# Optimization experiments

Hardware: AMD Instinct MI355X
Metric: run time of the kernel (lower is better)

Reference implementation:

```python
import jax, jax.numpy as jnp
import numpy as np

H = W = 256
FX = FY = 1.0
CX = CY = 0.5


def setup_inputs() -> dict:
    key = jax.random.key(0)
    k1, k2, k3 = jax.random.split(key, 3)
    B, N = 8, 500000
    points = jax.random.normal(k1, (B, N, 3), dtype=jnp.float32)
    densities = jax.random.uniform(k2, (B, N, 1), dtype=jnp.float32)
    depth = jax.random.uniform(k3, (B, 1, H, W), dtype=jnp.float32)
    return {"points": points, "densities": densities, "depth": depth}


def project_points_to_depth(points, densities):
    # points: [B,N,3], densities: [B,N,1] -> depth grid [B,1,H,W]
    B, N, _ = points.shape
    x = points[:, :, 0]
    y = points[:, :, 1]
    z = points[:, :, 2]
    # pinhole projection; .long() in torch truncates toward zero, as does astype(int32)
    u = jnp.clip(((FX * x / z + CX) * W).astype(jnp.int32), 0, W - 1)  # [B,N]
    v = jnp.clip(((FY * y / z + CY) * H).astype(jnp.int32), 0, H - 1)  # [B,N]
    d = densities[:, :, 0]
    val = jnp.where(d > 0.5, z * d, jnp.float32(0.0))  # conditional contribution
    idx = v * W + u  # flat pixel index [B,N]
    flat = jnp.zeros((B, H * W), dtype=points.dtype)
    flat = flat.at[jnp.arange(B)[:, None], idx].add(val)  # batched scatter-add
    return flat.reshape(B, 1, H, W)


def reference(points, densities, depth):
    projected = project_points_to_depth(points, densities)
    mask = projected > 0
    diff2 = jnp.where(mask, (projected - depth) ** 2, jnp.float32(0.0))
    count = jnp.maximum(jnp.sum(mask), 1)
    # F.mse_loss over masked elements == mean of squared diffs where mask
    return jnp.sum(diff2) / count.astype(diff2.dtype)
```

## Files before the change

### kernel.cpp

```cpp
#include <hip/hip_runtime.h>

#define HH 256
#define WW 256
#define HWSZ (HH * WW)

#define GRIDX 128
#define NSLOTS 1022

__global__ __launch_bounds__(256, 4) void scatter_k(
    const float* __restrict__ pts, const float* __restrict__ dens,
    float* __restrict__ flat, int N)
{
    __shared__ float lds[NSLOTS];
    for (int s = threadIdx.x; s < NSLOTS; s += 256) lds[s] = 0.0f;
    __syncthreads();

    int b = blockIdx.y;
    const float* pb = pts + (size_t)b * N * 3;
    const float* db = dens + (size_t)b * N;
    float* out = flat + (size_t)b * HWSZ;

    int ngroups = N >> 2;
    int gpb = (ngroups + GRIDX - 1) / GRIDX;
    int gbase = blockIdx.x * gpb;
    int gend = min(gbase + gpb, ngroups);
    int nit = (gpb + 255) >> 8;
    int last = ngroups - 1;
    const float4* p4 = (const float4*)pb;
    const float4* d4 = (const float4*)db;

    float corner[4] = {0.0f, 0.0f, 0.0f, 0.0f};

    auto proc = [&](const float4& a, const float4& bb, const float4& c,
                    const float4& dd) {
        float xs[4] = {a.x, a.w, bb.z, c.y};
        float ys[4] = {a.y, bb.x, bb.w, c.z};
        float zs[4] = {a.z, bb.y, c.x, c.w};
        float ds[4] = {dd.x, dd.y, dd.z, dd.w};

        #pragma unroll
        for (int k = 0; k < 4; k++) {
            float d = ds[k];
            float z = zs[k];
            bool acc = d > 0.5f;
            float r = __builtin_amdgcn_rcpf(z) * 256.0f;
            float uf = fmaf(xs[k], r, 128.0f);
            float vf = fmaf(ys[k], r, 128.0f);
            int u = (int)fminf(fmaxf(uf, 0.0f), 255.0f);
            int v = (int)fminf(fmaxf(vf, 0.0f), 255.0f);
            float val = z * d;

            bool u0 = (u == 0), u255 = (u == 255);
            bool v0 = (v == 0), v255 = (v == 255);
            bool ub = u0 | u255;
            bool vb = v0 | v255;
            bool iscorner = acc & ub & vb;
            bool isborder = acc & (ub ^ vb);
            bool isinter  = acc & !ub & !vb;

            int ci = (v255 ? 2 : 0) | (u255 ? 1 : 0);
            corner[0] += (iscorner && ci == 0) ? val : 0.0f;
            corner[1] += (iscorner && ci == 1) ? val : 0.0f;
            corner[2] += (iscorner && ci == 2) ? val : 0.0f;
            corner[3] += (iscorner && ci == 3) ? val : 0.0f;

            int slot = v0 ? u : (v255 ? 256 + u : (u0 ? 511 + v : 767 + v));
            if (isborder) atomicAdd(&lds[slot], val);
            if (isinter)  atomicAdd(out + v * WW + u, val);
        }
    };

    int g = gbase + threadIdx.x;
    int gc = min(g, last);
    float4 A  = p4[3 * gc];
    float4 Bv = p4[3 * gc + 1];
    float4 C  = p4[3 * gc + 2];
    float4 D  = d4[gc];
    if (g >= gend) { D.x = D.y = D.z = D.w = 0.0f; }

    for (int it = 0; it < nit; ++it) {
        int gn = g + 256;
        int gnc = min(gn, last);
        float4 nA  = p4[3 * gnc];
        float4 nB  = p4[3 * gnc + 1];
        float4 nC  = p4[3 * gnc + 2];
        float4 nD  = d4[gnc];
        if (gn >= gend) { nD.x = nD.y = nD.z = nD.w = 0.0f; }

        proc(A, Bv, C, D);

        A = nA; Bv = nB; C = nC; D = nD;
        g = gn;
    }

    #pragma unroll
    for (int j = 0; j < 4; j++) {
        float v = corner[j];
        #pragma unroll
        for (int off = 32; off > 0; off >>= 1) v += __shfl_down(v, off);
        if ((threadIdx.x & 63) == 0) {
            const int cslot[4] = {0, 255, 256, 511};
            atomicAdd(&lds[cslot[j]], v);
        }
    }

    __syncthreads();
    for (int s = threadIdx.x; s < NSLOTS; s += 256) {
        float v = lds[s];
        if (v != 0.0f) {
            int u, vv;
            if (s < 256)      { vv = 0;        u = s; }
            else if (s < 512) { vv = 255;      u = s - 256; }
            else if (s < 768) { u = 0;         vv = s - 512 + 1; }
            else              { u = 255;       vv = s - 768 + 1; }
            atomicAdd(out + vv * WW + u, v);
        }
    }
}

#define LBLOCKS 128
#define ELEMS_PER_THREAD 4
__global__ __launch_bounds__(256) void loss_k(
    const float* __restrict__ flat, const float* __restrict__ depth,
    float* __restrict__ accum, int* __restrict__ done,
    float* __restrict__ out, int total4, int nblocks)
{
    const float4* f4 = (const float4*)flat;
    const float4* z4 = (const float4*)depth;

    int i0 = blockIdx.x * blockDim.x + threadIdx.x;
    int stride = gridDim.x * blockDim.x;

    float4 p[ELEMS_PER_THREAD], q[ELEMS_PER_THREAD];
    bool ok[ELEMS_PER_THREAD];
    #pragma unroll
    for (int k = 0; k < ELEMS_PER_THREAD; k++) {
        int i = i0 + k * stride;
        ok[k] = i < total4;
        if (ok[k]) { p[k] = f4[i]; q[k] = z4[i]; }
    }
    float s = 0.0f;
    int c = 0;
    for (int i = i0 + ELEMS_PER_THREAD * stride; i < total4; i += stride) {
        float4 pp = f4[i];
        float4 qq = z4[i];
        if (pp.x > 0.0f) { float df = pp.x - qq.x; s += df * df; c++; }
        if (pp.y > 0.0f) { float df = pp.y - qq.y; s += df * df; c++; }
        if (pp.z > 0.0f) { float df = pp.z - qq.z; s += df * df; c++; }
        if (pp.w > 0.0f) { float df = pp.w - qq.w; s += df * df; c++; }
    }
    #pragma unroll
    for (int k = 0; k < ELEMS_PER_THREAD; k++) {
        if (ok[k]) {
            float4 pp = p[k], qq = q[k];
            if (pp.x > 0.0f) { float df = pp.x - qq.x; s += df * df; c++; }
            if (pp.y > 0.0f) { float df = pp.y - qq.y; s += df * df; c++; }
            if (pp.z > 0.0f) { float df = pp.z - qq.z; s += df * df; c++; }
            if (pp.w > 0.0f) { float df = pp.w - qq.w; s += df * df; c++; }
        }
    }

    #pragma unroll
    for (int off = 32; off > 0; off >>= 1) {
        s += __shfl_down(s, off);
        c += __shfl_down(c, off);
    }

    __shared__ float bsum[4];
    __shared__ int bcnt[4];
    int wave = threadIdx.x >> 6;
    if ((threadIdx.x & 63) == 0) { bsum[wave] = s; bcnt[wave] = c; }
    __syncthreads();
    if (threadIdx.x == 0) {
        float ts = bsum[0] + bsum[1] + bsum[2] + bsum[3];
        int tc = bcnt[0] + bcnt[1] + bcnt[2] + bcnt[3];
        atomicAdd(accum, ts);
        atomicAdd((int*)accum + 1, tc);
        __threadfence();
        int old = atomicAdd(done, 1);
        if (old == nblocks - 1) {
            float fs = atomicAdd(accum, 0.0f);
            int fc = atomicAdd((int*)accum + 1, 0);
            out[0] = fs / (float)(fc >= 1 ? fc : 1);
        }
    }
}

extern "C" void kernel_launch(void* const* d_in, const int* in_sizes, int n_in,
                              void* d_out, int out_size, void* d_ws, size_t ws_size,
                              hipStream_t stream) {
    const float* pts   = (const float*)d_in[0];
    const float* dens  = (const float*)d_in[1];
    const float* depth = (const float*)d_in[2];
    float* out = (float*)d_out;

    int B = in_sizes[2] / HWSZ;
    int N = in_sizes[0] / (3 * B);

    float* flat  = (float*)d_ws;
    float* accum = flat + (size_t)B * HWSZ;
    int*   done  = (int*)(accum + 16);

    hipMemsetAsync(d_ws, 0, ((size_t)B * HWSZ + 32) * sizeof(float), stream);

    dim3 sgrid(GRIDX, B);
    scatter_k<<<sgrid, 256, 0, stream>>>(pts, dens, flat, N);

    int total4 = B * HWSZ / 4;
    loss_k<<<dim3(LBLOCKS), 256, 0, stream>>>(flat, depth, accum, done, out,
                                              total4, LBLOCKS);
}
```

Before: 122.9 us.

## Fuse loss reduction into scatter kernel via per-batch tail blocks

Removes the separate loss kernel launch. The last TAILB blocks of each batch row spin-wait until all scatter blocks of that batch finish, then each computes the masked MSE over one slice of that batch's image, with a global counter for the final division. The block size also goes from 256 to 512 threads. This saves a launch and lets the loss of early-finishing batches overlap ongoing scatter work, at the cost of spin-waiting blocks that hold occupancy and depend on forward-progress assumptions, plus hardcoding B=8.

```diff
diff --git a/kernel.cpp b/kernel.cpp
--- a/kernel.cpp
+++ b/kernel.cpp
@@ -5,14 +5,19 @@
 #define HWSZ (HH * WW)
 
 #define GRIDX 128
+#define TPB 512
 #define NSLOTS 1022
-
-__global__ __launch_bounds__(256, 4) void scatter_k(
+#define TAILB 8
+
+__global__ __launch_bounds__(TPB, 8) void scatter_k(
     const float* __restrict__ pts, const float* __restrict__ dens,
-    float* __restrict__ flat, int N)
+    const float* __restrict__ depth, float* __restrict__ flat,
+    float* __restrict__ acc, int* __restrict__ dn,
+    float* __restrict__ outp, int N)
 {
     __shared__ float lds[NSLOTS];
-    for (int s = threadIdx.x; s < NSLOTS; s += 256) lds[s] = 0.0f;
+    __shared__ int sh_old;
+    for (int s = threadIdx.x; s < NSLOTS; s += TPB) lds[s] = 0.0f;
     __syncthreads();
 
     int b = blockIdx.y;
@@ -24,7 +29,7 @@
     int gpb = (ngroups + GRIDX - 1) / GRIDX;
     int gbase = blockIdx.x * gpb;
     int gend = min(gbase + gpb, ngroups);
-    int nit = (gpb + 255) >> 8;
+    int nit = (gpb + TPB - 1) / TPB;
     int last = ngroups - 1;
     const float4* p4 = (const float4*)pb;
     const float4* d4 = (const float4*)db;
@@ -42,7 +47,7 @@
         for (int k = 0; k < 4; k++) {
             float d = ds[k];
             float z = zs[k];
-            bool acc = d > 0.5f;
+            bool acc_ = d > 0.5f;
             float r = __builtin_amdgcn_rcpf(z) * 256.0f;
             float uf = fmaf(xs[k], r, 128.0f);
             float vf = fmaf(ys[k], r, 128.0f);
@@ -54,9 +59,9 @@
             bool v0 = (v == 0), v255 = (v == 255);
             bool ub = u0 | u255;
             bool vb = v0 | v255;
-            bool iscorner = acc & ub & vb;
-            bool isborder = acc & (ub ^ vb);
-            bool isinter  = acc & !ub & !vb;
+            bool iscorner = acc_ & ub & vb;
+            bool isborder = acc_ & (ub ^ vb);
+            bool isinter  = acc_ & !ub & !vb;
 
             int ci = (v255 ? 2 : 0) | (u255 ? 1 : 0);
             corner[0] += (iscorner && ci == 0) ? val : 0.0f;
@@ -79,12 +84,12 @@
     if (g >= gend) { D.x = D.y = D.z = D.w = 0.0f; }
 
     for (int it = 0; it < nit; ++it) {
-        int gn = g + 256;
+        int gn = g + TPB;
         int gnc = min(gn, last);
-        float4 nA  = p4[3 * gnc];
-        float4 nB  = p4[3 * gnc + 1];
-        float4 nC  = p4[3 * gnc + 2];
-        float4 nD  = d4[gnc];
+        float4 nA = p4[3 * gnc];
+        float4 nB = p4[3 * gnc + 1];
+        float4 nC = p4[3 * gnc + 2];
+        float4 nD = d4[gnc];
         if (gn >= gend) { nD.x = nD.y = nD.z = nD.w = 0.0f; }
 
         proc(A, Bv, C, D);
@@ -105,7 +110,7 @@
     }
 
     __syncthreads();
-    for (int s = threadIdx.x; s < NSLOTS; s += 256) {
+    for (int s = threadIdx.x; s < NSLOTS; s += TPB) {
         float v = lds[s];
         if (v != 0.0f) {
             int u, vv;
@@ -116,72 +121,60 @@
             atomicAdd(out + vv * WW + u, v);
         }
     }
-}
-
-#define LBLOCKS 128
-#define ELEMS_PER_THREAD 4
-__global__ __launch_bounds__(256) void loss_k(
-    const float* __restrict__ flat, const float* __restrict__ depth,
-    float* __restrict__ accum, int* __restrict__ done,
-    float* __restrict__ out, int total4, int nblocks)
-{
-    const float4* f4 = (const float4*)flat;
-    const float4* z4 = (const float4*)depth;
-
-    int i0 = blockIdx.x * blockDim.x + threadIdx.x;
-    int stride = gridDim.x * blockDim.x;
-
-    float4 p[ELEMS_PER_THREAD], q[ELEMS_PER_THREAD];
-    bool ok[ELEMS_PER_THREAD];
-    #pragma unroll
-    for (int k = 0; k < ELEMS_PER_THREAD; k++) {
-        int i = i0 + k * stride;
-        ok[k] = i < total4;
-        if (ok[k]) { p[k] = f4[i]; q[k] = z4[i]; }
-    }
+    __syncthreads();
+    if (threadIdx.x == 0) {
+        __threadfence();
+        sh_old = atomicAdd(&dn[b * 32], 1);
+    }
+    __syncthreads();
+    int old = sh_old;
+    if (old < GRIDX - TAILB) return;
+
+    if (old < GRIDX - 1) {
+        if (threadIdx.x == 0) {
+            while (__hip_atomic_load(&dn[b * 32], __ATOMIC_ACQUIRE,
+                                     __HIP_MEMORY_SCOPE_AGENT) < GRIDX)
+                __builtin_amdgcn_s_sleep(2);
+        }
+        __syncthreads();
+    }
+    int slice = old - (GRIDX - TAILB);
+    int base = b * HWSZ + slice * (HWSZ / TAILB);
     float s = 0.0f;
     int c = 0;
-    for (int i = i0 + ELEMS_PER_THREAD * stride; i < total4; i += stride) {
-        float4 pp = f4[i];
-        float4 qq = z4[i];
-        if (pp.x > 0.0f) { float df = pp.x - qq.x; s += df * df; c++; }
-        if (pp.y > 0.0f) { float df = pp.y - qq.y; s += df * df; c++; }
-        if (pp.z > 0.0f) { float df = pp.z - qq.z; s += df * df; c++; }
-        if (pp.w > 0.0f) { float df = pp.w - qq.w; s += df * df; c++; }
-    }
-    #pragma unroll
-    for (int k = 0; k < ELEMS_PER_THREAD; k++) {
-        if (ok[k]) {
-            float4 pp = p[k], qq = q[k];
-            if (pp.x > 0.0f) { float df = pp.x - qq.x; s += df * df; c++; }
-            if (pp.y > 0.0f) { float df = pp.y - qq.y; s += df * df; c++; }
-            if (pp.z > 0.0f) { float df = pp.z - qq.z; s += df * df; c++; }
-            if (pp.w > 0.0f) { float df = pp.w - qq.w; s += df * df; c++; }
-        }
-    }
-
+    #pragma unroll 4
+    for (int j = 0; j < (HWSZ / TAILB) / TPB; ++j) {
+        int idx = base + j * TPB + threadIdx.x;
+        float f = __hip_atomic_load(&flat[idx], __ATOMIC_RELAXED,
+                                    __HIP_MEMORY_SCOPE_AGENT);
+        float dq = depth[idx];
+        if (f > 0.0f) { float df = f - dq; s += df * df; c++; }
+    }
     #pragma unroll
     for (int off = 32; off > 0; off >>= 1) {
         s += __shfl_down(s, off);
         c += __shfl_down(c, off);
     }
-
-    __shared__ float bsum[4];
-    __shared__ int bcnt[4];
-    int wave = threadIdx.x >> 6;
-    if ((threadIdx.x & 63) == 0) { bsum[wave] = s; bcnt[wave] = c; }
+    __shared__ float bsum[TPB / 64];
+    __shared__ int bcnt[TPB / 64];
+    int wv = threadIdx.x >> 6;
+    if ((threadIdx.x & 63) == 0) { bsum[wv] = s; bcnt[wv] = c; }
     __syncthreads();
     if (threadIdx.x == 0) {
-        float ts = bsum[0] + bsum[1] + bsum[2] + bsum[3];
-        int tc = bcnt[0] + bcnt[1] + bcnt[2] + bcnt[3];
-        atomicAdd(accum, ts);
-        atomicAdd((int*)accum + 1, tc);
+        float ts = 0.0f; int tc = 0;
+        #pragma unroll
+        for (int i = 0; i < TPB / 64; i++) { ts += bsum[i]; tc += bcnt[i]; }
+        atomicAdd(&acc[b * 32], ts);
+        atomicAdd((int*)&acc[b * 32] + 1, tc);
         __threadfence();
-        int old = atomicAdd(done, 1);
-        if (old == nblocks - 1) {
-            float fs = atomicAdd(accum, 0.0f);
-            int fc = atomicAdd((int*)accum + 1, 0);
-            out[0] = fs / (float)(fc >= 1 ? fc : 1);
+        int o2 = atomicAdd(&dn[8 * 32], 1);
+        if (o2 == 8 * TAILB - 1) {
+            float fs = 0.0f; int fc = 0;
+            for (int bb = 0; bb < 8; bb++) {
+                fs += atomicAdd(&acc[bb * 32], 0.0f);
+                fc += atomicAdd((int*)&acc[bb * 32] + 1, 0);
+            }
+            outp[0] = fs / (float)(fc >= 1 ? fc : 1);
         }
     }
 }
@@ -197,16 +190,15 @@
     int B = in_sizes[2] / HWSZ;
     int N = in_sizes[0] / (3 * B);
 
-    float* flat  = (float*)d_ws;
-    float* accum = flat + (size_t)B * HWSZ;
-    int*   done  = (int*)(accum + 16);
-
-    hipMemsetAsync(d_ws, 0, ((size_t)B * HWSZ + 32) * sizeof(float), stream);
+    float* flat = (float*)d_ws;
+    float* acc  = flat + (size_t)B * HWSZ;
+    int*   dn   = (int*)(acc + 8 * 32);
+
+    hipMemsetAsync(d_ws, 0,
+                   ((size_t)B * HWSZ + 8 * 32 + 9 * 32) * sizeof(float),
+                   stream);
 
     dim3 sgrid(GRIDX, B);
-    scatter_k<<<sgrid, 256, 0, stream>>>(pts, dens, flat, N);
-
-    int total4 = B * HWSZ / 4;
-    loss_k<<<dim3(LBLOCKS), 256, 0, stream>>>(flat, depth, accum, done, out,
-                                              total4, LBLOCKS);
+    scatter_k<<<sgrid, TPB, 0, stream>>>(pts, dens, depth, flat, acc, dn,
+                                         out, N);
 }
```

Result: slower. 157.3 us (+28.0%).

## Issue all point loads upfront via inline asm and fully unroll scatter loop

Applied to the files above, without the earlier changes.

Replaces the one-ahead prefetch loop in the scatter kernel with a fixed four-iteration unrolled body. All sixteen vector loads are issued at once through inline global_load_dwordx4 asm, followed by a single waitcnt, so memory latency is paid once per thread. Launch bounds drop from 4 to 3 blocks per CU to leave room for the extra registers. It hardcodes exactly four groups per thread (N/4/128 = 977 ≤ 1024), so larger N would silently skip points.

```diff
diff --git a/kernel.cpp b/kernel.cpp
--- a/kernel.cpp
+++ b/kernel.cpp
@@ -7,7 +7,9 @@
 #define GRIDX 128
 #define NSLOTS 1022
 
-__global__ __launch_bounds__(256, 4) void scatter_k(
+typedef float vf4 __attribute__((ext_vector_type(4)));
+
+__global__ __launch_bounds__(256, 3) void scatter_k(
     const float* __restrict__ pts, const float* __restrict__ dens,
     float* __restrict__ flat, int N)
 {
@@ -24,15 +26,48 @@
     int gpb = (ngroups + GRIDX - 1) / GRIDX;
     int gbase = blockIdx.x * gpb;
     int gend = min(gbase + gpb, ngroups);
-    int nit = (gpb + 255) >> 8;
     int last = ngroups - 1;
-    const float4* p4 = (const float4*)pb;
-    const float4* d4 = (const float4*)db;
+    const vf4* p4 = (const vf4*)pb;
+    const vf4* d4 = (const vf4*)db;
+
+    int g0 = gbase + threadIdx.x;
+    int g1 = g0 + 256, g2 = g0 + 512, g3 = g0 + 768;
+    int c0 = min(g0, last), c1 = min(g1, last),
+        c2 = min(g2, last), c3 = min(g3, last);
+
+    const vf4* pa0 = p4 + 3 * c0; const vf4* pa1 = p4 + 3 * c1;
+    const vf4* pa2 = p4 + 3 * c2; const vf4* pa3 = p4 + 3 * c3;
+    const vf4* da0 = d4 + c0;     const vf4* da1 = d4 + c1;
+    const vf4* da2 = d4 + c2;     const vf4* da3 = d4 + c3;
+
+    vf4 A0, B0, C0, D0, A1, B1, C1, D1;
+    vf4 A2, B2, C2, D2, A3, B3, C3, D3;
+#define GLOAD(dst, base, off) \
+    asm volatile("global_load_dwordx4 %0, %1, off offset:" #off \
+                 : "=&v"(dst) : "v"(base) : "memory")
+    GLOAD(A0, pa0, 0); GLOAD(B0, pa0, 16); GLOAD(C0, pa0, 32);
+    GLOAD(A1, pa1, 0); GLOAD(B1, pa1, 16); GLOAD(C1, pa1, 32);
+    GLOAD(A2, pa2, 0); GLOAD(B2, pa2, 16); GLOAD(C2, pa2, 32);
+    GLOAD(A3, pa3, 0); GLOAD(B3, pa3, 16); GLOAD(C3, pa3, 32);
+    GLOAD(D0, da0, 0); GLOAD(D1, da1, 0);
+    GLOAD(D2, da2, 0); GLOAD(D3, da3, 0);
+#undef GLOAD
+    asm volatile("s_waitcnt vmcnt(0)"
+                 : "+v"(A0), "+v"(B0), "+v"(C0), "+v"(D0),
+                   "+v"(A1), "+v"(B1), "+v"(C1), "+v"(D1),
+                   "+v"(A2), "+v"(B2), "+v"(C2), "+v"(D2),
+                   "+v"(A3), "+v"(B3), "+v"(C3), "+v"(D3));
+    __builtin_amdgcn_sched_barrier(0);
+
+    if (g0 >= gend) { D0 = (vf4)0.0f; }
+    if (g1 >= gend) { D1 = (vf4)0.0f; }
+    if (g2 >= gend) { D2 = (vf4)0.0f; }
+    if (g3 >= gend) { D3 = (vf4)0.0f; }
 
     float corner[4] = {0.0f, 0.0f, 0.0f, 0.0f};
 
-    auto proc = [&](const float4& a, const float4& bb, const float4& c,
-                    const float4& dd) {
+    auto proc = [&](const vf4& a, const vf4& bb, const vf4& c,
+                    const vf4& dd) {
         float xs[4] = {a.x, a.w, bb.z, c.y};
         float ys[4] = {a.y, bb.x, bb.w, c.z};
         float zs[4] = {a.z, bb.y, c.x, c.w};
@@ -70,28 +105,10 @@
         }
     };
 
-    int g = gbase + threadIdx.x;
-    int gc = min(g, last);
-    float4 A  = p4[3 * gc];
-    float4 Bv = p4[3 * gc + 1];
-    float4 C  = p4[3 * gc + 2];
-    float4 D  = d4[gc];
-    if (g >= gend) { D.x = D.y = D.z = D.w = 0.0f; }
-
-    for (int it = 0; it < nit; ++it) {
-        int gn = g + 256;
-        int gnc = min(gn, last);
-        float4 nA  = p4[3 * gnc];
-        float4 nB  = p4[3 * gnc + 1];
-        float4 nC  = p4[3 * gnc + 2];
-        float4 nD  = d4[gnc];
-        if (gn >= gend) { nD.x = nD.y = nD.z = nD.w = 0.0f; }
-
-        proc(A, Bv, C, D);
-
-        A = nA; Bv = nB; C = nC; D = nD;
-        g = gn;
-    }
+    proc(A0, B0, C0, D0);
+    proc(A1, B1, C1, D1);
+    proc(A2, B2, C2, D2);
+    proc(A3, B3, C3, D3);
 
     #pragma unroll
     for (int j = 0; j < 4; j++) {
```

Measured after the change: 125.3 us. No clear change (+2.0%).
